# Optimization experiments

Hardware: AMD Instinct MI355X
Metric: run time of the kernel (lower is better)

## Reference

```python
import jax, jax.numpy as jnp
import numpy as np

B, C, V = 65536, 2, 3          # batch of coords, coord_dim, value_dim
D, K, S = 64, 1024, 4          # latent_dim, num_codes, num_latent_vectors (VQ stages)
H, L, F = 1024, 5, 25          # hidden_size, num_layers, num_freqs
IN = C * (2 * F + 1)           # 102: positional-encoded decoder input
COMMIT = 0.25


def setup_inputs() -> dict:
    key = jax.random.key(0)
    ks = jax.random.split(key, 12)
    coords = jax.random.uniform(ks[0], (B, C), jnp.float32, -1.0, 1.0)
    latents = jax.random.normal(ks[1], (1, S, D), jnp.float32)
    cb = jax.random.normal(ks[2], (S, K, D), jnp.float32)
    codebooks = cb / jnp.linalg.norm(cb, axis=-1, keepdims=True)  # unit-norm init as in module
    mod_W = jax.random.normal(ks[3], (L, D, H), jnp.float32) / np.sqrt(D)
    mod_b = jax.random.normal(ks[4], (L, H), jnp.float32) * 0.01
    dec_W0 = jax.random.normal(ks[5], (IN, H), jnp.float32) / np.sqrt(IN)
    dec_b0 = jax.random.normal(ks[6], (H,), jnp.float32) * 0.01
    dec_Wh = jax.random.normal(ks[7], (L - 1, H, H), jnp.float32) / np.sqrt(H)
    dec_bh = jax.random.normal(ks[8], (L - 1, H), jnp.float32) * 0.01
    dec_Wout = jax.random.normal(ks[9], (H, V), jnp.float32) / np.sqrt(H)
    dec_bout = jax.random.normal(ks[10], (V,), jnp.float32) * 0.01
    return dict(coords=coords, latent_idx=0, latents=latents, codebooks=codebooks,
                mod_W=mod_W, mod_b=mod_b, dec_W0=dec_W0, dec_b0=dec_b0,
                dec_Wh=dec_Wh, dec_bh=dec_bh, dec_Wout=dec_Wout, dec_bout=dec_bout)


def _vq(z, emb):
    # z: (1, D), emb: (K, D) -> squared-distance argmin + straight-through
    d = jnp.sum(z * z, axis=1, keepdims=True) - 2.0 * (z @ emb.T) + jnp.sum(emb * emb, axis=1)
    idx = jnp.argmin(d, axis=1)               # (1,)
    z_q = emb[idx]                            # (1, D)
    z_q_st = z_q + jax.lax.stop_gradient(z - z_q)   # fwd value == z, grad flows to embedding
    loss = COMMIT * jnp.mean((jax.lax.stop_gradient(z_q) - z) ** 2)
    return z_q_st, idx, loss


def reference(coords, latent_idx, latents, codebooks, mod_W, mod_b,
              dec_W0, dec_b0, dec_Wh, dec_bh, dec_Wout, dec_bout):
    img = latents[latent_idx]                 # (S, D)
    z_q_sum = jnp.zeros((1, D), coords.dtype)
    residual_target = jnp.zeros((1, D), coords.dtype)
    total_vq_loss = 0.0
    idxs = []
    for s in range(S):                        # residual VQ over fixed small #stages
        z_stage = img[s:s + 1]
        if s == 0:
            residual_target = z_stage
            z_cur = z_stage
        else:
            residual_target = residual_target + z_stage
            z_cur = residual_target - jax.lax.stop_gradient(z_q_sum)
        z_q_st, idx, l = _vq(z_cur, codebooks[s])
        z_q_sum = z_q_sum + z_q_st
        total_vq_loss = total_vq_loss + l
        idxs.append(idx)
    # modulation betas from the (same-for-all-rows) quantized latent; broadcast over B
    betas = jnp.einsum('od,ldh->loh', z_q_sum, mod_W) + mod_b[:, None, :]   # (L, 1, H)
    # positional encoding: [x, sin(pi*f0*x), cos(pi*f0*x), sin(pi*f1*x), ...]
    freqs = 2.0 ** jnp.arange(F, dtype=coords.dtype)
    ang = coords[:, None, :] * (freqs[None, :, None] * jnp.pi)              # (B, F, C)
    pe = jnp.concatenate(
        [coords, jnp.stack([jnp.sin(ang), jnp.cos(ang)], axis=2).reshape(coords.shape[0], -1)],
        axis=-1)                                                            # (B, IN)
    h = jax.nn.relu(pe @ dec_W0 + dec_b0 + betas[0])
    for i in range(L - 1):
        h = jax.nn.relu(h @ dec_Wh[i] + dec_bh[i] + betas[i + 1])
    values = h @ dec_Wout + dec_bout                                        # (B, V)
    return values, jnp.stack(idxs), total_vq_loss
```

## Files before the change

### kernel.cpp

```cpp
#include <hip/hip_runtime.h>
#include <hip/hip_bf16.h>
#include <stdint.h>

#define NB   65536
#define NC   2
#define NV   3
#define ND   64
#define NK   1024
#define NS   4
#define NH   1024
#define NL   5
#define NF   25
#define NIN  102
#define K0P  128

typedef float f32x4 __attribute__((ext_vector_type(4)));
typedef int   i32x4 __attribute__((ext_vector_type(4)));
typedef int   i32x8 __attribute__((ext_vector_type(8)));
typedef unsigned char u8;

__device__ __forceinline__ void load_lds16(const void* g, void* l) {
    __builtin_amdgcn_global_load_lds(
        (const __attribute__((address_space(1))) void*)g,
        (__attribute__((address_space(3))) void*)l,
        16, 0, 0);
}

__device__ __forceinline__ u8 to_fp8(float x) {
    return (u8)(__builtin_amdgcn_cvt_pk_fp8_f32(x, 0.0f, 0, false) & 0xff);
}


__global__ __launch_bounds__(1024) void vq_kernel(
    const float* __restrict__ latents, const int* __restrict__ latent_idx,
    const float* __restrict__ codebooks, float* __restrict__ zq_out,
    float* __restrict__ out) {
    __shared__ float zcur[ND], resid[ND], zqsum[ND], ssq[ND];
    __shared__ float sDw[16];
    __shared__ int   sKw[16];
    __shared__ int   sBest;
    int t = threadIdx.x, lane = t & 63, wv = t >> 6;
    const float* img = latents + (size_t)latent_idx[0] * (NS * ND);
    if (t < ND) { resid[t] = 0.f; zqsum[t] = 0.f; }
    __syncthreads();
    float lossAcc = 0.f;
    for (int s = 0; s < NS; s++) {
        if (t < ND) {
            float iv = img[s * ND + t];
            float r  = resid[t] + iv;
            resid[t] = r;
            zcur[t]  = (s == 0) ? iv : (r - zqsum[t]);
        }
        __syncthreads();
        float zz = 0.f;
#pragma unroll
        for (int d = 0; d < ND; d++) { float z = zcur[d]; zz += z * z; }
        const float4* e4 = (const float4*)(codebooks + ((size_t)s * NK + t) * ND);
        float dot = 0.f, ee = 0.f;
#pragma unroll
        for (int i = 0; i < 16; i++) {
            float4 v = e4[i];
            dot += zcur[4 * i + 0] * v.x; dot += zcur[4 * i + 1] * v.y;
            dot += zcur[4 * i + 2] * v.z; dot += zcur[4 * i + 3] * v.w;
            ee  += v.x * v.x; ee += v.y * v.y; ee += v.z * v.z; ee += v.w * v.w;
        }
        float dmin = zz - 2.0f * dot + ee;
        int   kmin = t;
#pragma unroll
        for (int m = 1; m < 64; m <<= 1) {
            float d2 = __shfl_xor(dmin, m);
            int   k2 = __shfl_xor(kmin, m);
            if (d2 < dmin || (d2 == dmin && k2 < kmin)) { dmin = d2; kmin = k2; }
        }
        if (lane == 0) { sDw[wv] = dmin; sKw[wv] = kmin; }
        __syncthreads();
        if (t == 0) {
            float bd = sDw[0]; int bk = sKw[0];
            for (int w = 1; w < 16; w++) {
                float d2 = sDw[w]; int k2 = sKw[w];
                if (d2 < bd || (d2 == bd && k2 < bk)) { bd = d2; bk = k2; }
            }
            sBest = bk;
            out[NB * NV + s] = (float)bk;
        }
        __syncthreads();
        int best = sBest;
        const float* eb = codebooks + ((size_t)s * NK + best) * ND;
        if (t < ND) {
            float zq = eb[t];
            float d  = zq - zcur[t];
            ssq[t]   = d * d;
            zqsum[t] = zqsum[t] + (zq + (zcur[t] - zq));
        }
        __syncthreads();
        if (t == 0) {
            float sum = 0.f;
            for (int d = 0; d < ND; d++) sum += ssq[d];
            lossAcc += 0.25f * (sum / (float)ND);
        }
    }
    if (t < ND) zq_out[t] = zqsum[t];
    if (t == 0) out[NB * NV + NS] = lossAcc;
}

__global__ __launch_bounds__(256) void betas_kernel(
    const float* __restrict__ zq, const float* __restrict__ mod_W,
    const float* __restrict__ mod_b, const float* __restrict__ b0,
    const float* __restrict__ bh, float* __restrict__ bb) {
    int g = blockIdx.x * 256 + threadIdx.x;
    int l = g >> 10, n = g & 1023;
    float acc = mod_b[g];
    for (int d = 0; d < ND; d++) acc += zq[d] * mod_W[(size_t)(l * ND + d) * NH + n];
    acc += (l == 0) ? b0[n] : bh[(size_t)(l - 1) * NH + n];
    bb[g] = acc;
}

__global__ __launch_bounds__(256) void init_out_kernel(
    const float* __restrict__ bout, float* __restrict__ out) {
    int g = blockIdx.x * 256 + threadIdx.x;
    out[g] = bout[g % NV];
}

__global__ __launch_bounds__(256) void prep_kernel(
    const float* __restrict__ src, u8* __restrict__ dst, int Ks, int Kp) {
    __shared__ float tile[32][33];
    int nIt = Kp >> 7;
    src += (size_t)blockIdx.z * Ks * NH;
    dst += (size_t)blockIdx.z * NH * Kp;
    int k0 = blockIdx.x * 32, n0 = blockIdx.y * 32;
    int tx = threadIdx.x, ty = threadIdx.y;
    for (int i = 0; i < 4; i++) {
        int k = k0 + ty + i * 8;
        int n = n0 + tx;
        tile[ty + i * 8][tx] = (k < Ks) ? src[(size_t)k * NH + n] : 0.0f;
    }
    __syncthreads();
    for (int i = 0; i < 4; i++) {
        int n = n0 + ty + i * 8;
        int k = k0 + tx;
        int bn = n >> 7, j = (n >> 4) & 7, r16 = n & 15;
        int it = k >> 7, q = (k >> 5) & 3, half = (k >> 4) & 1, b16 = k & 15;
        size_t flat = ((size_t)(((bn * nIt + it) * 8 + j) * 2 + half)) * 1024
                    + (q * 16 + r16) * 16 + b16;
        dst[flat] = to_fp8(tile[tx][ty + i * 8] * 64.0f);
    }
}

__device__ __forceinline__ float pe_val(const float* coords, int m, int k) {
    if (k < 2) return coords[m * 2 + k];
    if (k >= NIN) return 0.0f;
    int u = k - 2;
    int f = u >> 2, r = u & 3;
    float c = coords[m * 2 + (r & 1)];
    float a = c * __builtin_ldexpf(3.14159274101257324f, f);
    return (r < 2) ? sinf(a) : cosf(a);
}

__global__ __launch_bounds__(256) void pe_kernel(
    const float* __restrict__ coords, u8* __restrict__ pe) {
    int g = blockIdx.x * 256 + threadIdx.x;
    int m = g >> 5, k4 = (g & 31) * 4;
    float v0 = pe_val(coords, m, k4 + 0);
    float v1 = pe_val(coords, m, k4 + 1);
    float v2 = pe_val(coords, m, k4 + 2);
    float v3 = pe_val(coords, m, k4 + 3);
    int p = __builtin_amdgcn_cvt_pk_fp8_f32(v0, v1, 0, false);
    p     = __builtin_amdgcn_cvt_pk_fp8_f32(v2, v3, p, true);
    int m16 = m >> 4, r = m & 15, c32 = k4 >> 5, b = k4 & 31;
    *(int*)(pe + ((size_t)(m16 * 4 + c32) * 16 + r) * 32 + b) = p;
}

template <int MODE, int KT>
__global__ __launch_bounds__(256, 2) void gemm_kernel(
    const u8* __restrict__ A, const u8* __restrict__ W,
    const float* __restrict__ bb, u8* __restrict__ O,
    const float* __restrict__ Wout, float* __restrict__ out, int Mb) {
    __shared__ __align__(16) u8 smem[32768];
    u8* sW0 = smem;
    u8* sW1 = smem + 16384;
    int t   = threadIdx.x;
    int fid = blockIdx.x;
    int xcd = fid & 7;
    int j8  = fid >> 3;
    int bn  = j8 & 7;
    int bm  = xcd * (Mb >> 3) + (j8 >> 3);
    int lane = t & 63, wm = t >> 6;
    int q    = lane >> 4, r16 = lane & 15;
    const int nIt = KT >> 7;

    const u8* wslab = W + (size_t)(bn * nIt) * 16384;
    const u8* abase = A + ((size_t)(bm * 16 + wm * 4) * (KT >> 5)) * 512 + lane * 32;

    f32x4 acc[4][8];
    f32x4 zero = {0.f, 0.f, 0.f, 0.f};
    for (int i = 0; i < 4; i++)
        for (int j = 0; j < 8; j++) acc[i][j] = zero;

#pragma unroll
    for (int p = 0; p < 4; p++) {
        int g = p * 256 + t;
        load_lds16((const void*)(wslab + g * 16), (void*)(sW0 + g * 16));
    }
    i32x8 afc[4], afn[4];
#pragma unroll
    for (int i = 0; i < 4; i++) {
        const u8* p = abase + ((size_t)i * (KT >> 5)) * 512;
        i32x4 lo = *(const i32x4*)(p);
        i32x4 hi = *(const i32x4*)(p + 16);
        afc[i] = __builtin_shufflevector(lo, hi, 0, 1, 2, 3, 4, 5, 6, 7);
    }
    __syncthreads();

#pragma unroll 1
    for (int it = 0; it < nIt; it++) {
        u8* bufc = (it & 1) ? sW1 : sW0;
        u8* bufn = (it & 1) ? sW0 : sW1;
        if (it + 1 < nIt) {
            const u8* ws = wslab + (size_t)(it + 1) * 16384;
#pragma unroll
            for (int p = 0; p < 4; p++) {
                int g = p * 256 + t;
                load_lds16((const void*)(ws + g * 16), (void*)(bufn + g * 16));
            }
#pragma unroll
            for (int i = 0; i < 4; i++) {
                const u8* p = abase + ((size_t)i * (KT >> 5) + (it + 1) * 4) * 512;
                i32x4 lo = *(const i32x4*)(p);
                i32x4 hi = *(const i32x4*)(p + 16);
                afn[i] = __builtin_shufflevector(lo, hi, 0, 1, 2, 3, 4, 5, 6, 7);
            }
        }
#pragma unroll
        for (int j = 0; j < 8; j++) {
            i32x4 lo = *(const i32x4*)(bufc + j * 2048 + lane * 16);
            i32x4 hi = *(const i32x4*)(bufc + j * 2048 + 1024 + lane * 16);
            i32x8 bfr = __builtin_shufflevector(lo, hi, 0, 1, 2, 3, 4, 5, 6, 7);
#pragma unroll
            for (int i = 0; i < 4; i++)
                acc[i][j] = __builtin_amdgcn_mfma_scale_f32_16x16x128_f8f6f4(
                    bfr, afc[i], acc[i][j], 0, 0,
                    0, 0x79797979,
                    0, 0x7f7f7f7f);
        }
        __syncthreads();
#pragma unroll
        for (int i = 0; i < 4; i++) afc[i] = afn[i];
    }

    if constexpr (MODE == 0) {
        u8* eb = smem;
#pragma unroll
        for (int i = 0; i < 4; i++) {
#pragma unroll
            for (int j = 0; j < 8; j++) {
                int nl = j * 16 + q * 4;
                f32x4 b4 = *(const f32x4*)(bb + bn * 128 + nl);
                float v0 = fmaxf(acc[i][j][0] + b4[0], 0.0f);
                float v1 = fmaxf(acc[i][j][1] + b4[1], 0.0f);
                float v2 = fmaxf(acc[i][j][2] + b4[2], 0.0f);
                float v3 = fmaxf(acc[i][j][3] + b4[3], 0.0f);
                int p = __builtin_amdgcn_cvt_pk_fp8_f32(v0, v1, 0, false);
                p     = __builtin_amdgcn_cvt_pk_fp8_f32(v2, v3, p, true);
                int idx = (((wm * 4 + i) * 4 + (j >> 1)) * 16 + r16) * 32
                        + (j & 1) * 16 + q * 4;
                *(int*)(eb + idx) = p;
            }
        }
        __syncthreads();
#pragma unroll
        for (int rd = 0; rd < 8; rd++) {
            int g2  = rd * 256 + t;
            int seg = g2 >> 5, off = (g2 & 31) * 16;
            int m16l = seg >> 2, c32l = seg & 3;
            i32x4 v = *(const i32x4*)(eb + seg * 512 + off);
            *(i32x4*)(O + ((size_t)((bm * 16 + m16l) * 32 + bn * 4 + c32l)) * 512 + off) = v;
        }
    } else {
#pragma unroll
        for (int i = 0; i < 4; i++) {
            float p0 = 0.f, p1 = 0.f, p2 = 0.f;
#pragma unroll
            for (int j = 0; j < 8; j++) {
                int nb = bn * 128 + j * 16 + q * 4;
                f32x4 b4 = *(const f32x4*)(bb + nb);
#pragma unroll
                for (int r = 0; r < 4; r++) {
                    float val = fmaxf(acc[i][j][r] + b4[r], 0.0f);
                    const float* w = Wout + (size_t)(nb + r) * NV;
                    p0 += val * w[0]; p1 += val * w[1]; p2 += val * w[2];
                }
            }
            p0 += __shfl_xor(p0, 16); p0 += __shfl_xor(p0, 32);
            p1 += __shfl_xor(p1, 16); p1 += __shfl_xor(p1, 32);
            p2 += __shfl_xor(p2, 16); p2 += __shfl_xor(p2, 32);
            if (q == 0) {
                int m = bm * 256 + wm * 64 + i * 16 + r16;
                atomicAdd(&out[(size_t)m * NV + 0], p0);
                atomicAdd(&out[(size_t)m * NV + 1], p1);
                atomicAdd(&out[(size_t)m * NV + 2], p2);
            }
        }
    }
}

extern "C" void kernel_launch(void* const* d_in, const int* in_sizes, int n_in,
                              void* d_out, int out_size, void* d_ws, size_t ws_size,
                              hipStream_t stream) {
    const float* coords     = (const float*)d_in[0];
    const int*   latent_idx = (const int*)d_in[1];
    const float* latents    = (const float*)d_in[2];
    const float* codebooks  = (const float*)d_in[3];
    const float* mod_W      = (const float*)d_in[4];
    const float* mod_b      = (const float*)d_in[5];
    const float* dec_W0     = (const float*)d_in[6];
    const float* dec_b0     = (const float*)d_in[7];
    const float* dec_Wh     = (const float*)d_in[8];
    const float* dec_bh     = (const float*)d_in[9];
    const float* dec_Wout   = (const float*)d_in[10];
    const float* dec_bout   = (const float*)d_in[11];
    float* out = (float*)d_out;

    char* wsb = (char*)d_ws;
    float* zq  = (float*)(wsb + 0);
    float* bb  = (float*)(wsb + 256);
    u8*    W0T = (u8*)(wsb + 20736);
    u8*    WhT = (u8*)(wsb + 151808);
    const size_t fixed_end = 4346368;

    int Bc = 65536;
    while (Bc > 2048 && fixed_end + 2 * (size_t)Bc * NH > ws_size)
        Bc >>= 1;
    int Mb = Bc / 256;

    u8* hA = (u8*)(wsb + fixed_end);
    u8* hB = hA + (size_t)Bc * NH;
    u8* pe = hB;

    vq_kernel<<<1, 1024, 0, stream>>>(latents, latent_idx, codebooks, zq, out);
    betas_kernel<<<20, 256, 0, stream>>>(zq, mod_W, mod_b, dec_b0, dec_bh, bb);
    init_out_kernel<<<(NB * NV) / 256, 256, 0, stream>>>(dec_bout, out);
    prep_kernel<<<dim3(4, 32, 1), dim3(32, 8), 0, stream>>>(dec_W0, W0T, NIN, K0P);
    prep_kernel<<<dim3(32, 32, 4), dim3(32, 8), 0, stream>>>(dec_Wh, WhT, NH, NH);

    for (int c0 = 0; c0 < NB; c0 += Bc) {
        pe_kernel<<<(Bc * 32) / 256, 256, 0, stream>>>(coords + (size_t)c0 * NC, pe);
        gemm_kernel<0, K0P><<<8 * Mb, 256, 0, stream>>>(
            pe, W0T, bb + 0 * NH, hA, nullptr, nullptr, Mb);
        gemm_kernel<0, NH><<<8 * Mb, 256, 0, stream>>>(
            hA, WhT + 0 * (size_t)NH * NH, bb + 1 * NH, hB, nullptr, nullptr, Mb);
        gemm_kernel<0, NH><<<8 * Mb, 256, 0, stream>>>(
            hB, WhT + 1 * (size_t)NH * NH, bb + 2 * NH, hA, nullptr, nullptr, Mb);
        gemm_kernel<0, NH><<<8 * Mb, 256, 0, stream>>>(
            hA, WhT + 2 * (size_t)NH * NH, bb + 3 * NH, hB, nullptr, nullptr, Mb);
        gemm_kernel<1, NH><<<8 * Mb, 256, 0, stream>>>(
            hB, WhT + 3 * (size_t)NH * NH, bb + 4 * NH, nullptr,
            dec_Wout, out + (size_t)c0 * NV, Mb);
    }
}
```

Baseline: 486.8 us.

## Split GEMM tile across 8 waves with new activation layout and reduced accumulators

The GEMM block grows from 256 to 512 threads, with each wave computing a 64x64 sub-tile (4x4 accumulators) instead of 64x128, which halves accumulator registers to allow more waves per CU. The activation fp8 layout is changed so that each lane's 32-byte operand comes from two 16-byte chunks 1024 bytes apart, and the pe and epilogue writers are updated to match. The A prefetch into registers is dropped, so A is loaded directly each iteration, and the K loop is fully unrolled. The final layer now combines the two N-half partials in LDS before issuing atomics, halving atomic traffic. In exchange, each weight tile read from LDS is shared by fewer MFMAs, and A load latency is no longer hidden by a prefetch.

Measured after the change: 846.1 us. 73.8% more time.

```diff
diff --git a/kernel.cpp b/kernel.cpp
--- a/kernel.cpp
+++ b/kernel.cpp
@@ -28,6 +28,13 @@
 
 __device__ __forceinline__ u8 to_fp8(float x) {
     return (u8)(__builtin_amdgcn_cvt_pk_fp8_f32(x, 0.0f, 0, false) & 0xff);
+}
+
+__device__ __forceinline__ f32x4 mfma128(i32x8 wf, i32x8 af, f32x4 c) {
+    return __builtin_amdgcn_mfma_scale_f32_16x16x128_f8f6f4(
+        wf, af, c, 0, 0,
+        0, 0x79797979,
+        0, 0x7f7f7f7f);
 }
 
 
@@ -166,94 +173,105 @@
     float v3 = pe_val(coords, m, k4 + 3);
     int p = __builtin_amdgcn_cvt_pk_fp8_f32(v0, v1, 0, false);
     p     = __builtin_amdgcn_cvt_pk_fp8_f32(v2, v3, p, true);
-    int m16 = m >> 4, r = m & 15, c32 = k4 >> 5, b = k4 & 31;
-    *(int*)(pe + ((size_t)(m16 * 4 + c32) * 16 + r) * 32 + b) = p;
+    int m16 = m >> 4, r16 = m & 15;
+    int q = k4 >> 5, half = (k4 >> 4) & 1, b16 = k4 & 15;
+    *(int*)(pe + ((size_t)(m16 * 2 + half)) * 1024 + (q * 16 + r16) * 16 + b16) = p;
 }
 
 template <int MODE, int KT>
-__global__ __launch_bounds__(256, 2) void gemm_kernel(
+__global__ __launch_bounds__(512, 4) void gemm_kernel(
     const u8* __restrict__ A, const u8* __restrict__ W,
     const float* __restrict__ bb, u8* __restrict__ O,
     const float* __restrict__ Wout, float* __restrict__ out, int Mb) {
     __shared__ __align__(16) u8 smem[32768];
-    u8* sW0 = smem;
-    u8* sW1 = smem + 16384;
     int t   = threadIdx.x;
     int fid = blockIdx.x;
     int xcd = fid & 7;
     int j8  = fid >> 3;
     int bn  = j8 & 7;
     int bm  = xcd * (Mb >> 3) + (j8 >> 3);
-    int lane = t & 63, wm = t >> 6;
+    int lane = t & 63, w = t >> 6;
+    int wm4  = w >> 1, wn = w & 1;
     int q    = lane >> 4, r16 = lane & 15;
-    const int nIt = KT >> 7;
+    constexpr int nIt = KT >> 7;
 
     const u8* wslab = W + (size_t)(bn * nIt) * 16384;
-    const u8* abase = A + ((size_t)(bm * 16 + wm * 4) * (KT >> 5)) * 512 + lane * 32;
-
-    f32x4 acc[4][8];
+    const u8* abase = A + (size_t)(bm * 16 + wm4 * 4) * (nIt * 2048) + lane * 16;
+
+    f32x4 acc[4][4];
     f32x4 zero = {0.f, 0.f, 0.f, 0.f};
+#pragma unroll
     for (int i = 0; i < 4; i++)
-        for (int j = 0; j < 8; j++) acc[i][j] = zero;
-
-#pragma unroll
-    for (int p = 0; p < 4; p++) {
-        int g = p * 256 + t;
-        load_lds16((const void*)(wslab + g * 16), (void*)(sW0 + g * 16));
-    }
-    i32x8 afc[4], afn[4];
-#pragma unroll
-    for (int i = 0; i < 4; i++) {
-        const u8* p = abase + ((size_t)i * (KT >> 5)) * 512;
-        i32x4 lo = *(const i32x4*)(p);
-        i32x4 hi = *(const i32x4*)(p + 16);
-        afc[i] = __builtin_shufflevector(lo, hi, 0, 1, 2, 3, 4, 5, 6, 7);
-    }
+#pragma unroll
+        for (int j = 0; j < 4; j++) acc[i][j] = zero;
+
+#define STAGE_W(IT)                                                            \
+    {                                                                          \
+        u8* dst_ = smem + ((IT) & 1) * 16384;                                  \
+        load_lds16((const void*)(wslab + (size_t)(IT) * 16384 + t * 16),       \
+                   (void*)(dst_ + t * 16));                                    \
+        load_lds16((const void*)(wslab + (size_t)(IT) * 16384 + 8192 + t * 16),\
+                   (void*)(dst_ + 8192 + t * 16));                             \
+    }
+#define LDPAIR_L(dst, base)                                                    \
+    {                                                                          \
+        i32x4 lo_ = *(const i32x4*)(base);                                     \
+        i32x4 hi_ = *(const i32x4*)((base) + 1024);                            \
+        dst = __builtin_shufflevector(lo_, hi_, 0, 1, 2, 3, 4, 5, 6, 7);       \
+    }
+
+    STAGE_W(0)
     __syncthreads();
 
-#pragma unroll 1
+#pragma unroll
     for (int it = 0; it < nIt; it++) {
-        u8* bufc = (it & 1) ? sW1 : sW0;
-        u8* bufn = (it & 1) ? sW0 : sW1;
-        if (it + 1 < nIt) {
-            const u8* ws = wslab + (size_t)(it + 1) * 16384;
-#pragma unroll
-            for (int p = 0; p < 4; p++) {
-                int g = p * 256 + t;
-                load_lds16((const void*)(ws + g * 16), (void*)(bufn + g * 16));
-            }
-#pragma unroll
-            for (int i = 0; i < 4; i++) {
-                const u8* p = abase + ((size_t)i * (KT >> 5) + (it + 1) * 4) * 512;
-                i32x4 lo = *(const i32x4*)(p);
-                i32x4 hi = *(const i32x4*)(p + 16);
-                afn[i] = __builtin_shufflevector(lo, hi, 0, 1, 2, 3, 4, 5, 6, 7);
-            }
-        }
-#pragma unroll
-        for (int j = 0; j < 8; j++) {
-            i32x4 lo = *(const i32x4*)(bufc + j * 2048 + lane * 16);
-            i32x4 hi = *(const i32x4*)(bufc + j * 2048 + 1024 + lane * 16);
-            i32x8 bfr = __builtin_shufflevector(lo, hi, 0, 1, 2, 3, 4, 5, 6, 7);
-#pragma unroll
-            for (int i = 0; i < 4; i++)
-                acc[i][j] = __builtin_amdgcn_mfma_scale_f32_16x16x128_f8f6f4(
-                    bfr, afc[i], acc[i][j], 0, 0,
-                    0, 0x79797979,
-                    0, 0x7f7f7f7f);
-        }
-        __syncthreads();
-#pragma unroll
-        for (int i = 0; i < 4; i++) afc[i] = afn[i];
-    }
+        if (it + 1 < nIt) STAGE_W(it + 1)
+
+        i32x8 a0, a1, a2, a3;
+        LDPAIR_L(a0, abase + (size_t)(0 * nIt + it) * 2048)
+        LDPAIR_L(a1, abase + (size_t)(1 * nIt + it) * 2048)
+        LDPAIR_L(a2, abase + (size_t)(2 * nIt + it) * 2048)
+        LDPAIR_L(a3, abase + (size_t)(3 * nIt + it) * 2048)
+
+        const u8* Wb = smem + (it & 1) * 16384;
+        {
+            i32x8 w0, w1;
+            LDPAIR_L(w0, Wb + (wn * 4 + 0) * 2048 + lane * 16)
+            LDPAIR_L(w1, Wb + (wn * 4 + 1) * 2048 + lane * 16)
+            acc[0][0] = mfma128(w0, a0, acc[0][0]);
+            acc[1][0] = mfma128(w0, a1, acc[1][0]);
+            acc[2][0] = mfma128(w0, a2, acc[2][0]);
+            acc[3][0] = mfma128(w0, a3, acc[3][0]);
+            acc[0][1] = mfma128(w1, a0, acc[0][1]);
+            acc[1][1] = mfma128(w1, a1, acc[1][1]);
+            acc[2][1] = mfma128(w1, a2, acc[2][1]);
+            acc[3][1] = mfma128(w1, a3, acc[3][1]);
+        }
+        {
+            i32x8 w2, w3;
+            LDPAIR_L(w2, Wb + (wn * 4 + 2) * 2048 + lane * 16)
+            LDPAIR_L(w3, Wb + (wn * 4 + 3) * 2048 + lane * 16)
+            acc[0][2] = mfma128(w2, a0, acc[0][2]);
+            acc[1][2] = mfma128(w2, a1, acc[1][2]);
+            acc[2][2] = mfma128(w2, a2, acc[2][2]);
+            acc[3][2] = mfma128(w2, a3, acc[3][2]);
+            acc[0][3] = mfma128(w3, a0, acc[0][3]);
+            acc[1][3] = mfma128(w3, a1, acc[1][3]);
+            acc[2][3] = mfma128(w3, a2, acc[2][3]);
+            acc[3][3] = mfma128(w3, a3, acc[3][3]);
+        }
+        __syncthreads();
+    }
+#undef STAGE_W
+#undef LDPAIR_L
 
     if constexpr (MODE == 0) {
         u8* eb = smem;
 #pragma unroll
         for (int i = 0; i < 4; i++) {
 #pragma unroll
-            for (int j = 0; j < 8; j++) {
-                int nl = j * 16 + q * 4;
+            for (int j = 0; j < 4; j++) {
+                int nl = (wn * 4 + j) * 16 + q * 4;
                 f32x4 b4 = *(const f32x4*)(bb + bn * 128 + nl);
                 float v0 = fmaxf(acc[i][j][0] + b4[0], 0.0f);
                 float v1 = fmaxf(acc[i][j][1] + b4[1], 0.0f);
@@ -261,44 +279,55 @@
                 float v3 = fmaxf(acc[i][j][3] + b4[3], 0.0f);
                 int p = __builtin_amdgcn_cvt_pk_fp8_f32(v0, v1, 0, false);
                 p     = __builtin_amdgcn_cvt_pk_fp8_f32(v2, v3, p, true);
-                int idx = (((wm * 4 + i) * 4 + (j >> 1)) * 16 + r16) * 32
-                        + (j & 1) * 16 + q * 4;
+                int m16l = wm4 * 4 + i;
+                int half = j & 1;
+                int qp   = wn * 2 + (j >> 1);
+                int idx  = (m16l * 2 + half) * 1024 + (qp * 16 + r16) * 16 + q * 4;
                 *(int*)(eb + idx) = p;
             }
         }
         __syncthreads();
 #pragma unroll
-        for (int rd = 0; rd < 8; rd++) {
-            int g2  = rd * 256 + t;
-            int seg = g2 >> 5, off = (g2 & 31) * 16;
-            int m16l = seg >> 2, c32l = seg & 3;
-            i32x4 v = *(const i32x4*)(eb + seg * 512 + off);
-            *(i32x4*)(O + ((size_t)((bm * 16 + m16l) * 32 + bn * 4 + c32l)) * 512 + off) = v;
+        for (int rd = 0; rd < 4; rd++) {
+            int g2 = rd * 512 + t;
+            i32x4 v = *(const i32x4*)(eb + g2 * 16);
+            *(i32x4*)(O + ((size_t)((bm * 16 + (g2 >> 7)) * 8 + bn)) * 2048
+                      + (g2 & 127) * 16) = v;
         }
     } else {
+        float* red = (float*)smem;
 #pragma unroll
         for (int i = 0; i < 4; i++) {
             float p0 = 0.f, p1 = 0.f, p2 = 0.f;
 #pragma unroll
-            for (int j = 0; j < 8; j++) {
-                int nb = bn * 128 + j * 16 + q * 4;
+            for (int j = 0; j < 4; j++) {
+                int nb = bn * 128 + (wn * 4 + j) * 16 + q * 4;
                 f32x4 b4 = *(const f32x4*)(bb + nb);
 #pragma unroll
                 for (int r = 0; r < 4; r++) {
                     float val = fmaxf(acc[i][j][r] + b4[r], 0.0f);
-                    const float* w = Wout + (size_t)(nb + r) * NV;
-                    p0 += val * w[0]; p1 += val * w[1]; p2 += val * w[2];
+                    const float* wo = Wout + (size_t)(nb + r) * NV;
+                    p0 += val * wo[0]; p1 += val * wo[1]; p2 += val * wo[2];
                 }
             }
             p0 += __shfl_xor(p0, 16); p0 += __shfl_xor(p0, 32);
             p1 += __shfl_xor(p1, 16); p1 += __shfl_xor(p1, 32);
             p2 += __shfl_xor(p2, 16); p2 += __shfl_xor(p2, 32);
             if (q == 0) {
-                int m = bm * 256 + wm * 64 + i * 16 + r16;
-                atomicAdd(&out[(size_t)m * NV + 0], p0);
-                atomicAdd(&out[(size_t)m * NV + 1], p1);
-                atomicAdd(&out[(size_t)m * NV + 2], p2);
+                int row = (wm4 * 4 + i) * 16 + r16;
+                int base = (row * 2 + wn) * 3;
+                red[base + 0] = p0; red[base + 1] = p1; red[base + 2] = p2;
             }
+        }
+        __syncthreads();
+        if (t < 256) {
+            float s0 = red[(t * 2 + 0) * 3 + 0] + red[(t * 2 + 1) * 3 + 0];
+            float s1 = red[(t * 2 + 0) * 3 + 1] + red[(t * 2 + 1) * 3 + 1];
+            float s2 = red[(t * 2 + 0) * 3 + 2] + red[(t * 2 + 1) * 3 + 2];
+            int m = bm * 256 + t;
+            atomicAdd(&out[(size_t)m * NV + 0], s0);
+            atomicAdd(&out[(size_t)m * NV + 1], s1);
+            atomicAdd(&out[(size_t)m * NV + 2], s2);
         }
     }
 }
@@ -344,15 +373,15 @@
 
     for (int c0 = 0; c0 < NB; c0 += Bc) {
         pe_kernel<<<(Bc * 32) / 256, 256, 0, stream>>>(coords + (size_t)c0 * NC, pe);
-        gemm_kernel<0, K0P><<<8 * Mb, 256, 0, stream>>>(
+        gemm_kernel<0, K0P><<<8 * Mb, 512, 0, stream>>>(
             pe, W0T, bb + 0 * NH, hA, nullptr, nullptr, Mb);
-        gemm_kernel<0, NH><<<8 * Mb, 256, 0, stream>>>(
+        gemm_kernel<0, NH><<<8 * Mb, 512, 0, stream>>>(
             hA, WhT + 0 * (size_t)NH * NH, bb + 1 * NH, hB, nullptr, nullptr, Mb);
-        gemm_kernel<0, NH><<<8 * Mb, 256, 0, stream>>>(
+        gemm_kernel<0, NH><<<8 * Mb, 512, 0, stream>>>(
             hB, WhT + 1 * (size_t)NH * NH, bb + 2 * NH, hA, nullptr, nullptr, Mb);
-        gemm_kernel<0, NH><<<8 * Mb, 256, 0, stream>>>(
+        gemm_kernel<0, NH><<<8 * Mb, 512, 0, stream>>>(
             hA, WhT + 2 * (size_t)NH * NH, bb + 3 * NH, hB, nullptr, nullptr, Mb);
-        gemm_kernel<1, NH><<<8 * Mb, 256, 0, stream>>>(
+        gemm_kernel<1, NH><<<8 * Mb, 512, 0, stream>>>(
             hB, WhT + 3 * (size_t)NH * NH, bb + 4 * NH, nullptr,
             dec_Wout, out + (size_t)c0 * NV, Mb);
     }
```

## Process two K-slabs per iteration with 64KB double-buffered LDS weights

Applied to the files above, without the earlier changes.

Restructures the FP8 GEMM main loop so each iteration loads and consumes two 16KB weight slabs (32KB per buffer, 64KB total LDS), halving the number of barriers and loop iterations. A-fragment loads are interleaved between the two MFMA slabs to overlap global latency with compute, and the single-slab case (layer 0) gets its own path. The larger LDS footprint may limit two blocks per CU, and the paired loop assumes an even number of K iterations whenever there is more than one.

New measurement: 784.2 us. 1.61x slower.

```diff
diff --git a/kernel.cpp b/kernel.cpp
--- a/kernel.cpp
+++ b/kernel.cpp
@@ -175,9 +175,7 @@
     const u8* __restrict__ A, const u8* __restrict__ W,
     const float* __restrict__ bb, u8* __restrict__ O,
     const float* __restrict__ Wout, float* __restrict__ out, int Mb) {
-    __shared__ __align__(16) u8 smem[32768];
-    u8* sW0 = smem;
-    u8* sW1 = smem + 16384;
+    __shared__ __align__(16) u8 smem[65536];
     int t   = threadIdx.x;
     int fid = blockIdx.x;
     int xcd = fid & 7;
@@ -186,7 +184,7 @@
     int bm  = xcd * (Mb >> 3) + (j8 >> 3);
     int lane = t & 63, wm = t >> 6;
     int q    = lane >> 4, r16 = lane & 15;
-    const int nIt = KT >> 7;
+    constexpr int nIt = KT >> 7;
 
     const u8* wslab = W + (size_t)(bn * nIt) * 16384;
     const u8* abase = A + ((size_t)(bm * 16 + wm * 4) * (KT >> 5)) * 512 + lane * 32;
@@ -196,56 +194,79 @@
     for (int i = 0; i < 4; i++)
         for (int j = 0; j < 8; j++) acc[i][j] = zero;
 
-#pragma unroll
-    for (int p = 0; p < 4; p++) {
-        int g = p * 256 + t;
-        load_lds16((const void*)(wslab + g * 16), (void*)(sW0 + g * 16));
-    }
-    i32x8 afc[4], afn[4];
-#pragma unroll
-    for (int i = 0; i < 4; i++) {
-        const u8* p = abase + ((size_t)i * (KT >> 5)) * 512;
-        i32x4 lo = *(const i32x4*)(p);
-        i32x4 hi = *(const i32x4*)(p + 16);
-        afc[i] = __builtin_shufflevector(lo, hi, 0, 1, 2, 3, 4, 5, 6, 7);
-    }
-    __syncthreads();
+#define LOAD_AFRAG(dst, IT)                                                    \
+    {                                                                          \
+        _Pragma("unroll")                                                      \
+        for (int i = 0; i < 4; i++) {                                          \
+            const u8* p = abase + ((size_t)i * (KT >> 5) + (IT) * 4) * 512;    \
+            i32x4 lo = *(const i32x4*)(p);                                     \
+            i32x4 hi = *(const i32x4*)(p + 16);                                \
+            dst[i] = __builtin_shufflevector(lo, hi, 0, 1, 2, 3, 4, 5, 6, 7);  \
+        }                                                                      \
+    }
+#define MFMA_SLAB(base, af)                                                    \
+    {                                                                          \
+        _Pragma("unroll")                                                      \
+        for (int j = 0; j < 8; j++) {                                          \
+            i32x4 lo = *(const i32x4*)((base) + j * 2048 + lane * 16);         \
+            i32x4 hi = *(const i32x4*)((base) + j * 2048 + 1024 + lane * 16);  \
+            i32x8 bfr = __builtin_shufflevector(lo, hi, 0, 1, 2, 3, 4, 5, 6, 7);\
+            _Pragma("unroll")                                                  \
+            for (int i = 0; i < 4; i++)                                        \
+                acc[i][j] = __builtin_amdgcn_mfma_scale_f32_16x16x128_f8f6f4(  \
+                    bfr, af[i], acc[i][j], 0, 0,                               \
+                    0, 0x79797979,                   \
+                    0, 0x7f7f7f7f);                  \
+        }                                                                      \
+    }
+
+    if constexpr (nIt == 1) {
+#pragma unroll
+        for (int p = 0; p < 4; p++) {
+            int g = p * 256 + t;
+            load_lds16((const void*)(wslab + g * 16), (void*)(smem + g * 16));
+        }
+        i32x8 afA[4];
+        LOAD_AFRAG(afA, 0)
+        __syncthreads();
+        MFMA_SLAB(smem, afA)
+        __syncthreads();
+    } else {
+        i32x8 afA[4], afB[4];
+        LOAD_AFRAG(afA, 0)
+        asm volatile("" ::: "memory");
+#pragma unroll
+        for (int p = 0; p < 8; p++) {
+            int g = p * 256 + t;
+            load_lds16((const void*)(wslab + g * 16), (void*)(smem + g * 16));
+        }
+        __syncthreads();
 
 #pragma unroll 1
-    for (int it = 0; it < nIt; it++) {
-        u8* bufc = (it & 1) ? sW1 : sW0;
-        u8* bufn = (it & 1) ? sW0 : sW1;
-        if (it + 1 < nIt) {
-            const u8* ws = wslab + (size_t)(it + 1) * 16384;
-#pragma unroll
-            for (int p = 0; p < 4; p++) {
-                int g = p * 256 + t;
-                load_lds16((const void*)(ws + g * 16), (void*)(bufn + g * 16));
-            }
-#pragma unroll
-            for (int i = 0; i < 4; i++) {
-                const u8* p = abase + ((size_t)i * (KT >> 5) + (it + 1) * 4) * 512;
-                i32x4 lo = *(const i32x4*)(p);
-                i32x4 hi = *(const i32x4*)(p + 16);
-                afn[i] = __builtin_shufflevector(lo, hi, 0, 1, 2, 3, 4, 5, 6, 7);
-            }
-        }
-#pragma unroll
-        for (int j = 0; j < 8; j++) {
-            i32x4 lo = *(const i32x4*)(bufc + j * 2048 + lane * 16);
-            i32x4 hi = *(const i32x4*)(bufc + j * 2048 + 1024 + lane * 16);
-            i32x8 bfr = __builtin_shufflevector(lo, hi, 0, 1, 2, 3, 4, 5, 6, 7);
-#pragma unroll
-            for (int i = 0; i < 4; i++)
-                acc[i][j] = __builtin_amdgcn_mfma_scale_f32_16x16x128_f8f6f4(
-                    bfr, afc[i], acc[i][j], 0, 0,
-                    0, 0x79797979,
-                    0, 0x7f7f7f7f);
-        }
-        __syncthreads();
-#pragma unroll
-        for (int i = 0; i < 4; i++) afc[i] = afn[i];
-    }
+        for (int pr = 0; pr < nIt / 2; pr++) {
+            u8* bufc = smem + ((pr & 1) ? 32768 : 0);
+            u8* bufn = smem + ((pr & 1) ? 0 : 32768);
+            int it0 = 2 * pr;
+            LOAD_AFRAG(afB, it0 + 1)
+            asm volatile("" ::: "memory");
+            if (pr + 1 < nIt / 2) {
+                const u8* ws = wslab + (size_t)(it0 + 2) * 16384;
+#pragma unroll
+                for (int p = 0; p < 8; p++) {
+                    int g = p * 256 + t;
+                    load_lds16((const void*)(ws + g * 16), (void*)(bufn + g * 16));
+                }
+            }
+            MFMA_SLAB(bufc, afA)
+            if (pr + 1 < nIt / 2) {
+                LOAD_AFRAG(afA, it0 + 2)
+            }
+            MFMA_SLAB(bufc + 16384, afB)
+            __syncthreads();
+        }
+    }
+#undef LOAD_AFRAG
+#undef MFMA_SLAB
 
     if constexpr (MODE == 0) {
         u8* eb = smem;
```

## Switch FP8 GEMMs to 32x32x64 scaled MFMA with matching operand layouts

Applied to the files above, without the earlier changes.

Replaces the 16x16x128 scaled FP8 MFMA tiles with 32x32x64 tiles. The weight prep, positional-encoding and inter-layer activation layouts are rearranged to feed the new instruction's operand format. The per-wave tile stays 64x128, but each B fragment read from LDS is now reused across fewer, larger MFMAs, cutting LDS reads per flop and the number of MFMA issues. It also adds a single-iteration path for the first layer. The risk is that any mismatch between the three rewritten layouts and the epilogue indexing would corrupt results.

Result: faster. 466.6 us (-4.1%).

```diff
diff --git a/kernel.cpp b/kernel.cpp
--- a/kernel.cpp
+++ b/kernel.cpp
@@ -14,9 +14,10 @@
 #define NIN  102
 #define K0P  128
 
-typedef float f32x4 __attribute__((ext_vector_type(4)));
-typedef int   i32x4 __attribute__((ext_vector_type(4)));
-typedef int   i32x8 __attribute__((ext_vector_type(8)));
+typedef float f32x4  __attribute__((ext_vector_type(4)));
+typedef float f32x16 __attribute__((ext_vector_type(16)));
+typedef int   i32x4  __attribute__((ext_vector_type(4)));
+typedef int   i32x8  __attribute__((ext_vector_type(8)));
 typedef unsigned char u8;
 
 __device__ __forceinline__ void load_lds16(const void* g, void* l) {
@@ -28,6 +29,13 @@
 
 __device__ __forceinline__ u8 to_fp8(float x) {
     return (u8)(__builtin_amdgcn_cvt_pk_fp8_f32(x, 0.0f, 0, false) & 0xff);
+}
+
+__device__ __forceinline__ f32x16 mfma32(i32x8 wf, i32x8 af, f32x16 c) {
+    return __builtin_amdgcn_mfma_scale_f32_32x32x64_f8f6f4(
+        wf, af, c, 0, 0,
+        0, 0x79797979,
+        0, 0x7f7f7f7f);
 }
 
 
@@ -124,7 +132,6 @@
 __global__ __launch_bounds__(256) void prep_kernel(
     const float* __restrict__ src, u8* __restrict__ dst, int Ks, int Kp) {
     __shared__ float tile[32][33];
-    int nIt = Kp >> 7;
     src += (size_t)blockIdx.z * Ks * NH;
     dst += (size_t)blockIdx.z * NH * Kp;
     int k0 = blockIdx.x * 32, n0 = blockIdx.y * 32;
@@ -138,10 +145,10 @@
     for (int i = 0; i < 4; i++) {
         int n = n0 + ty + i * 8;
         int k = k0 + tx;
-        int bn = n >> 7, j = (n >> 4) & 7, r16 = n & 15;
-        int it = k >> 7, q = (k >> 5) & 3, half = (k >> 4) & 1, b16 = k & 15;
-        size_t flat = ((size_t)(((bn * nIt + it) * 8 + j) * 2 + half)) * 1024
-                    + (q * 16 + r16) * 16 + b16;
+        int bn = n >> 7, j32 = (n >> 5) & 3, r32 = n & 31;
+        int ks = k >> 6, kh = (k >> 5) & 1, h = (k >> 4) & 1, b16 = k & 15;
+        size_t flat = (size_t)bn * ((size_t)Kp * 128)
+                    + ((size_t)(((ks * 4 + j32) * 2 + h) * 2 + kh) * 32 + r32) * 16 + b16;
         dst[flat] = to_fp8(tile[tx][ty + i * 8] * 64.0f);
     }
 }
@@ -166,8 +173,10 @@
     float v3 = pe_val(coords, m, k4 + 3);
     int p = __builtin_amdgcn_cvt_pk_fp8_f32(v0, v1, 0, false);
     p     = __builtin_amdgcn_cvt_pk_fp8_f32(v2, v3, p, true);
-    int m16 = m >> 4, r = m & 15, c32 = k4 >> 5, b = k4 & 31;
-    *(int*)(pe + ((size_t)(m16 * 4 + c32) * 16 + r) * 32 + b) = p;
+    int m32 = m >> 5, r32 = m & 31;
+    int ks = k4 >> 6, kh = (k4 >> 5) & 1, h = (k4 >> 4) & 1, b16 = k4 & 15;
+    *(int*)(pe + (size_t)(m32 * 2 + ks) * 2048
+            + ((h * 2 + kh) * 32 + r32) * 16 + b16) = p;
 }
 
 template <int MODE, int KT>
@@ -176,8 +185,6 @@
     const float* __restrict__ bb, u8* __restrict__ O,
     const float* __restrict__ Wout, float* __restrict__ out, int Mb) {
     __shared__ __align__(16) u8 smem[32768];
-    u8* sW0 = smem;
-    u8* sW1 = smem + 16384;
     int t   = threadIdx.x;
     int fid = blockIdx.x;
     int xcd = fid & 7;
@@ -185,116 +192,150 @@
     int bn  = j8 & 7;
     int bm  = xcd * (Mb >> 3) + (j8 >> 3);
     int lane = t & 63, wm = t >> 6;
-    int q    = lane >> 4, r16 = lane & 15;
-    const int nIt = KT >> 7;
-
-    const u8* wslab = W + (size_t)(bn * nIt) * 16384;
-    const u8* abase = A + ((size_t)(bm * 16 + wm * 4) * (KT >> 5)) * 512 + lane * 32;
-
-    f32x4 acc[4][8];
-    f32x4 zero = {0.f, 0.f, 0.f, 0.f};
-    for (int i = 0; i < 4; i++)
-        for (int j = 0; j < 8; j++) acc[i][j] = zero;
-
-#pragma unroll
-    for (int p = 0; p < 4; p++) {
-        int g = p * 256 + t;
-        load_lds16((const void*)(wslab + g * 16), (void*)(sW0 + g * 16));
-    }
-    i32x8 afc[4], afn[4];
-#pragma unroll
-    for (int i = 0; i < 4; i++) {
-        const u8* p = abase + ((size_t)i * (KT >> 5)) * 512;
-        i32x4 lo = *(const i32x4*)(p);
-        i32x4 hi = *(const i32x4*)(p + 16);
-        afc[i] = __builtin_shufflevector(lo, hi, 0, 1, 2, 3, 4, 5, 6, 7);
-    }
-    __syncthreads();
+    int r32  = lane & 31, hl = lane >> 5;
+    constexpr int nIt = KT >> 7;
+    constexpr int nKs = KT >> 6;
+
+    const u8* wslab = W + (size_t)bn * ((size_t)KT * 128);
+    const u8* abase = A + ((size_t)(bm * 8 + wm * 2) * nKs) * 2048 + lane * 16;
+
+    f32x16 acc[2][4];
+#pragma unroll
+    for (int i = 0; i < 2; i++)
+#pragma unroll
+        for (int j = 0; j < 4; j++)
+#pragma unroll
+            for (int e = 0; e < 16; e++) acc[i][j][e] = 0.0f;
+
+#define LOAD_AF(dst, KS)                                                       \
+    {                                                                          \
+        _Pragma("unroll")                                                      \
+        for (int mt = 0; mt < 2; mt++) {                                       \
+            const u8* p = abase + ((size_t)mt * nKs + (KS)) * 2048;            \
+            i32x4 lo = *(const i32x4*)(p);                                     \
+            i32x4 hi = *(const i32x4*)(p + 1024);                              \
+            dst[mt] = __builtin_shufflevector(lo, hi, 0, 1, 2, 3, 4, 5, 6, 7); \
+        }                                                                      \
+    }
+#define MFMA_HALF(base, KSL, AF)                                               \
+    {                                                                          \
+        _Pragma("unroll")                                                      \
+        for (int j = 0; j < 4; j++) {                                          \
+            const u8* c = (base) + (KSL) * 8192 + j * 2048 + lane * 16;        \
+            i32x4 lo = *(const i32x4*)(c);                                     \
+            i32x4 hi = *(const i32x4*)(c + 1024);                              \
+            i32x8 wf = __builtin_shufflevector(lo, hi, 0, 1, 2, 3, 4, 5, 6, 7);\
+            acc[0][j] = mfma32(wf, AF[0], acc[0][j]);                          \
+            acc[1][j] = mfma32(wf, AF[1], acc[1][j]);                          \
+        }                                                                      \
+    }
+
+    if constexpr (nIt == 1) {
+#pragma unroll
+        for (int p = 0; p < 4; p++) {
+            int g = p * 256 + t;
+            load_lds16((const void*)(wslab + g * 16), (void*)(smem + g * 16));
+        }
+        i32x8 af0[2], af1[2];
+        LOAD_AF(af0, 0)
+        LOAD_AF(af1, 1)
+        __syncthreads();
+        MFMA_HALF(smem, 0, af0)
+        MFMA_HALF(smem, 1, af1)
+        __syncthreads();
+    } else {
+#pragma unroll
+        for (int p = 0; p < 4; p++) {
+            int g = p * 256 + t;
+            load_lds16((const void*)(wslab + g * 16), (void*)(smem + g * 16));
+        }
+        i32x8 afc0[2], afc1[2], afn0[2], afn1[2];
+        LOAD_AF(afc0, 0)
+        LOAD_AF(afc1, 1)
+        __syncthreads();
 
 #pragma unroll 1
-    for (int it = 0; it < nIt; it++) {
-        u8* bufc = (it & 1) ? sW1 : sW0;
-        u8* bufn = (it & 1) ? sW0 : sW1;
-        if (it + 1 < nIt) {
-            const u8* ws = wslab + (size_t)(it + 1) * 16384;
-#pragma unroll
-            for (int p = 0; p < 4; p++) {
-                int g = p * 256 + t;
-                load_lds16((const void*)(ws + g * 16), (void*)(bufn + g * 16));
+        for (int it = 0; it < nIt; it++) {
+            u8* bufc = smem + ((it & 1) ? 16384 : 0);
+            u8* bufn = smem + ((it & 1) ? 0 : 16384);
+            if (it + 1 < nIt) {
+                const u8* ws = wslab + (size_t)(it + 1) * 16384;
+#pragma unroll
+                for (int p = 0; p < 4; p++) {
+                    int g = p * 256 + t;
+                    load_lds16((const void*)(ws + g * 16), (void*)(bufn + g * 16));
+                }
+                LOAD_AF(afn0, 2 * (it + 1))
+                LOAD_AF(afn1, 2 * (it + 1) + 1)
             }
-#pragma unroll
-            for (int i = 0; i < 4; i++) {
-                const u8* p = abase + ((size_t)i * (KT >> 5) + (it + 1) * 4) * 512;
-                i32x4 lo = *(const i32x4*)(p);
-                i32x4 hi = *(const i32x4*)(p + 16);
-                afn[i] = __builtin_shufflevector(lo, hi, 0, 1, 2, 3, 4, 5, 6, 7);
-            }
-        }
-#pragma unroll
-        for (int j = 0; j < 8; j++) {
-            i32x4 lo = *(const i32x4*)(bufc + j * 2048 + lane * 16);
-            i32x4 hi = *(const i32x4*)(bufc + j * 2048 + 1024 + lane * 16);
-            i32x8 bfr = __builtin_shufflevector(lo, hi, 0, 1, 2, 3, 4, 5, 6, 7);
-#pragma unroll
-            for (int i = 0; i < 4; i++)
-                acc[i][j] = __builtin_amdgcn_mfma_scale_f32_16x16x128_f8f6f4(
-                    bfr, afc[i], acc[i][j], 0, 0,
-                    0, 0x79797979,
-                    0, 0x7f7f7f7f);
-        }
-        __syncthreads();
-#pragma unroll
-        for (int i = 0; i < 4; i++) afc[i] = afn[i];
-    }
+            MFMA_HALF(bufc, 0, afc0)
+            MFMA_HALF(bufc, 1, afc1)
+            __syncthreads();
+#pragma unroll
+            for (int mt = 0; mt < 2; mt++) { afc0[mt] = afn0[mt]; afc1[mt] = afn1[mt]; }
+        }
+    }
+#undef LOAD_AF
+#undef MFMA_HALF
 
     if constexpr (MODE == 0) {
         u8* eb = smem;
 #pragma unroll
-        for (int i = 0; i < 4; i++) {
-#pragma unroll
-            for (int j = 0; j < 8; j++) {
-                int nl = j * 16 + q * 4;
-                f32x4 b4 = *(const f32x4*)(bb + bn * 128 + nl);
-                float v0 = fmaxf(acc[i][j][0] + b4[0], 0.0f);
-                float v1 = fmaxf(acc[i][j][1] + b4[1], 0.0f);
-                float v2 = fmaxf(acc[i][j][2] + b4[2], 0.0f);
-                float v3 = fmaxf(acc[i][j][3] + b4[3], 0.0f);
-                int p = __builtin_amdgcn_cvt_pk_fp8_f32(v0, v1, 0, false);
-                p     = __builtin_amdgcn_cvt_pk_fp8_f32(v2, v3, p, true);
-                int idx = (((wm * 4 + i) * 4 + (j >> 1)) * 16 + r16) * 32
-                        + (j & 1) * 16 + q * 4;
-                *(int*)(eb + idx) = p;
+        for (int mt = 0; mt < 2; mt++) {
+#pragma unroll
+            for (int nt = 0; nt < 4; nt++) {
+                int kh  = nt & 1;
+                int seg = (wm * 2 + mt) * 2 + (nt >> 1);
+#pragma unroll
+                for (int g = 0; g < 4; g++) {
+                    int nbase = nt * 32 + 8 * g + 4 * hl;
+                    f32x4 b4 = *(const f32x4*)(bb + bn * 128 + nbase);
+                    float v0 = fmaxf(acc[mt][nt][4 * g + 0] + b4[0], 0.0f);
+                    float v1 = fmaxf(acc[mt][nt][4 * g + 1] + b4[1], 0.0f);
+                    float v2 = fmaxf(acc[mt][nt][4 * g + 2] + b4[2], 0.0f);
+                    float v3 = fmaxf(acc[mt][nt][4 * g + 3] + b4[3], 0.0f);
+                    int p = __builtin_amdgcn_cvt_pk_fp8_f32(v0, v1, 0, false);
+                    p     = __builtin_amdgcn_cvt_pk_fp8_f32(v2, v3, p, true);
+                    int h   = g >> 1;
+                    int idx = seg * 2048 + ((h * 2 + kh) * 32 + r32) * 16
+                            + ((8 * g + 4 * hl) & 15);
+                    *(int*)(eb + idx) = p;
+                }
             }
         }
         __syncthreads();
 #pragma unroll
         for (int rd = 0; rd < 8; rd++) {
             int g2  = rd * 256 + t;
-            int seg = g2 >> 5, off = (g2 & 31) * 16;
-            int m16l = seg >> 2, c32l = seg & 3;
-            i32x4 v = *(const i32x4*)(eb + seg * 512 + off);
-            *(i32x4*)(O + ((size_t)((bm * 16 + m16l) * 32 + bn * 4 + c32l)) * 512 + off) = v;
+            int seg = g2 >> 7, off = (g2 & 127) * 16;
+            int m32l = seg >> 1, ksl = seg & 1;
+            i32x4 v = *(const i32x4*)(eb + seg * 2048 + off);
+            *(i32x4*)(O + ((size_t)((bm * 8 + m32l) * (NH >> 6) + bn * 2 + ksl)) * 2048
+                      + off) = v;
         }
     } else {
 #pragma unroll
-        for (int i = 0; i < 4; i++) {
+        for (int mt = 0; mt < 2; mt++) {
             float p0 = 0.f, p1 = 0.f, p2 = 0.f;
 #pragma unroll
-            for (int j = 0; j < 8; j++) {
-                int nb = bn * 128 + j * 16 + q * 4;
-                f32x4 b4 = *(const f32x4*)(bb + nb);
-#pragma unroll
-                for (int r = 0; r < 4; r++) {
-                    float val = fmaxf(acc[i][j][r] + b4[r], 0.0f);
-                    const float* w = Wout + (size_t)(nb + r) * NV;
-                    p0 += val * w[0]; p1 += val * w[1]; p2 += val * w[2];
+            for (int nt = 0; nt < 4; nt++) {
+#pragma unroll
+                for (int g = 0; g < 4; g++) {
+                    int nbase = bn * 128 + nt * 32 + 8 * g + 4 * hl;
+                    f32x4 b4 = *(const f32x4*)(bb + nbase);
+#pragma unroll
+                    for (int rr = 0; rr < 4; rr++) {
+                        float val = fmaxf(acc[mt][nt][4 * g + rr] + b4[rr], 0.0f);
+                        const float* wo = Wout + (size_t)(nbase + rr) * NV;
+                        p0 += val * wo[0]; p1 += val * wo[1]; p2 += val * wo[2];
+                    }
                 }
             }
-            p0 += __shfl_xor(p0, 16); p0 += __shfl_xor(p0, 32);
-            p1 += __shfl_xor(p1, 16); p1 += __shfl_xor(p1, 32);
-            p2 += __shfl_xor(p2, 16); p2 += __shfl_xor(p2, 32);
-            if (q == 0) {
-                int m = bm * 256 + wm * 64 + i * 16 + r16;
+            p0 += __shfl_xor(p0, 32);
+            p1 += __shfl_xor(p1, 32);
+            p2 += __shfl_xor(p2, 32);
+            if (hl == 0) {
+                int m = bm * 256 + wm * 64 + mt * 32 + r32;
                 atomicAdd(&out[(size_t)m * NV + 0], p0);
                 atomicAdd(&out[(size_t)m * NV + 1], p1);
                 atomicAdd(&out[(size_t)m * NV + 2], p2);
```
